# Optimization experiments

Hardware: AMD Instinct MI355X
Metric: run time of the kernel (lower is better)

The kernel has to match this reference:

```python
import jax, jax.numpy as jnp
import numpy as np

DIM = 512
HEADS = 8
DIM_HEAD = 64  # default dim_head used for scale, matches DIM//HEADS here
SCALE = DIM_HEAD ** -0.5
B, X, Y = 8, 32, 32


def setup_inputs() -> dict:
    key = jax.random.key(0)
    k0, k1, k2, k3 = jax.random.split(key, 4)
    fmap = jax.random.normal(k0, (B, DIM, X, Y), dtype=jnp.float32)
    # 1x1 convs as matrices: weight [out, in]
    Wqkvl = jax.random.normal(k1, (4 * DIM, DIM), dtype=jnp.float32) * (DIM ** -0.5)
    Wout = jax.random.normal(k2, (DIM, DIM), dtype=jnp.float32) * (DIM ** -0.5)
    bout = jax.random.normal(k3, (DIM,), dtype=jnp.float32) * 0.01
    return {"fmap": fmap, "Wqkvl": Wqkvl, "Wout": Wout, "bout": bout}


def reference(fmap, Wqkvl, Wout, bout):
    b, c, x, y = fmap.shape
    h, d = HEADS, c // HEADS
    n = x * y
    # 1x1 conv projection to q,k,v,L
    qkvL = jnp.einsum('oc,bcxy->boxy', Wqkvl, fmap)  # [b, 4c, x, y]
    q, k, v, L = jnp.split(qkvL, 4, axis=1)
    # 'b (h d) x y -> b h (x y) d'
    def to_tokens(t):
        return t.reshape(b, h, d, n).transpose(0, 1, 3, 2)
    q, k, v, L = map(to_tokens, (q, k, v, L))
    dots = jnp.einsum('bhid,bhjd->bhij', q, k) * SCALE  # [b,h,n,n]
    attn = jax.nn.softmax(dots, axis=-1)
    out = jnp.einsum('bhij,bhjd->bhid', attn, v) + L  # [b,h,n,d]
    # 'b h (x y) d -> b (h d) x y'
    out = out.transpose(0, 1, 3, 2).reshape(b, c, x, y)
    # output 1x1 conv with bias (dropout=0 -> identity)
    out = jnp.einsum('oc,bcxy->boxy', Wout, out) + bout[None, :, None, None]
    return out
```

## Files before the change

kernel.cpp:

```cpp
#include <hip/hip_runtime.h>

#define Bn 8
#define Cn 512
#define Hn 8
#define Dn 64
#define Nn 1024
#define SCALEQ 0.125f

typedef unsigned short u16;
typedef unsigned short u16x8 __attribute__((ext_vector_type(8)));
typedef unsigned short u16x4 __attribute__((ext_vector_type(4)));
typedef short s16x4 __attribute__((ext_vector_type(4)));
typedef float f32x4 __attribute__((ext_vector_type(4)));
typedef __bf16 bf16x8 __attribute__((ext_vector_type(8)));

__device__ __forceinline__ u16 f2bf(float f){
  unsigned u = __float_as_uint(f);
  u += 0x7fffu + ((u >> 16) & 1u);
  return (u16)(u >> 16);
}
__device__ __forceinline__ float bf2f(u16 h){
  return __uint_as_float(((unsigned)h) << 16);
}
__device__ __forceinline__ f32x4 mfma16(u16x8 a, u16x8 b, f32x4 c){
  return __builtin_amdgcn_mfma_f32_16x16x32_bf16(
      __builtin_bit_cast(bf16x8, a), __builtin_bit_cast(bf16x8, b), c, 0, 0, 0);
}
__device__ __forceinline__ f32x4 mfma16k16(u16x4 a, u16x4 b, f32x4 c){
  return __builtin_amdgcn_mfma_f32_16x16x16bf16_1k(
      __builtin_bit_cast(s16x4, a), __builtin_bit_cast(s16x4, b), c, 0, 0, 0);
}

__device__ __forceinline__ void gload16(const u16* src, u16* dst){
  __builtin_amdgcn_global_load_lds(
      (const __attribute__((address_space(1))) unsigned int*)src,
      (__attribute__((address_space(3))) unsigned int*)dst, 16, 0, 0);
}

__global__ __launch_bounds__(256) void k_convert(const float* __restrict__ src,
                                                 u16* __restrict__ dst, int n4){
  int i = blockIdx.x * 256 + threadIdx.x;
  if (i >= n4) return;
  float4 f = reinterpret_cast<const float4*>(src)[i];
  u16x4 o;
  o[0] = f2bf(f.x); o[1] = f2bf(f.y); o[2] = f2bf(f.z); o[3] = f2bf(f.w);
  reinterpret_cast<u16x4*>(dst)[i] = o;
}

__global__ __launch_bounds__(256) void k_transpose(const float* __restrict__ fmap,
                                                   u16* __restrict__ fmapT){
  __shared__ float tile[32][33];
  const int n0 = blockIdx.x * 32, c0 = blockIdx.y * 32, b = blockIdx.z;
  const int tx = threadIdx.x & 31, ty = threadIdx.x >> 5;
  const float* src = fmap + ((size_t)b * Cn + c0) * Nn + n0;
#pragma unroll
  for (int i = 0; i < 4; i++) tile[ty + 8*i][tx] = src[(size_t)(ty + 8*i) * Nn + tx];
  __syncthreads();
  u16* dst = fmapT + ((size_t)b * Nn + n0) * Cn + c0;
#pragma unroll
  for (int i = 0; i < 4; i++) dst[(size_t)(ty + 8*i) * Cn + tx] = f2bf(tile[tx][ty + 8*i]);
}

__device__ __forceinline__ void stage64(const u16* g, size_t ldg, u16* lbase, int w, int lane){
#pragma unroll
  for (int s = 0; s < 2; s++){
    int row = s*32 + w*8 + (lane>>3);
    const u16* src = g + (size_t)row*ldg + (((lane&7) ^ (row&7)) * 8);
    u16* dst = lbase + (s*32 + w*8)*64;
    gload16(src, dst);
  }
}
__device__ __forceinline__ void stage128x32(const u16* g, size_t ldg, u16* lbase, int w, int lane){
#pragma unroll
  for (int s = 0; s < 2; s++){
    int row = s*64 + w*16 + (lane>>2);
    const u16* src = g + (size_t)row*ldg + (((lane&3) ^ (row&3)) * 8);
    u16* dst = lbase + (s*64 + w*16)*32;
    gload16(src, dst);
  }
}

__device__ __forceinline__ void gemm_fma(const u16x8 (&af)[4], const u16x8 (&bf)[4],
                                         f32x4 (&acc)[4][4]){
#pragma unroll
  for (int i = 0; i < 4; i++)
#pragma unroll
    for (int j = 0; j < 4; j++)
      acc[i][j] = mfma16(af[i], bf[j], acc[i][j]);
}

__device__ __forceinline__ void gemm_nt_128(const u16* __restrict__ Ap, int lda,
                                            const u16* __restrict__ Bp, int ldb,
                                            u16* sA, u16* sB,
                                            f32x4 (&acc)[4][4]){
  const int tid = threadIdx.x;
  const int w = tid >> 6, lane = tid & 63, r = lane & 15, g = lane >> 4;
  const int wi = w >> 1, wj = w & 1;
  stage128x32(Ap, lda, sA, w, lane);
  stage128x32(Bp, ldb, sB, w, lane);
  for (int ks = 0; ks < Cn/32; ks++){
    __syncthreads();
    const int cur = ks & 1;
    if (ks + 1 < Cn/32){
      stage128x32(Ap + (ks+1)*32, lda, sA + (cur^1)*128*32, w, lane);
      stage128x32(Bp + (ks+1)*32, ldb, sB + (cur^1)*128*32, w, lane);
    }
    const u16* Al = sA + cur*128*32;
    const u16* Bl = sB + cur*128*32;
    u16x8 af[4], bf[4];
#pragma unroll
    for (int t = 0; t < 4; t++){
      int ar = wi*64 + t*16 + r;
      af[t] = *reinterpret_cast<const u16x8*>(&Al[ar*32 + ((g ^ (ar&3)) * 8)]);
      int br = wj*64 + t*16 + r;
      bf[t] = *reinterpret_cast<const u16x8*>(&Bl[br*32 + ((g ^ (br&3)) * 8)]);
    }
    gemm_fma(af, bf, acc);
  }
}

__global__ __launch_bounds__(256) void k_gemm1(const u16* __restrict__ fmapT,
                                               const u16* __restrict__ W1,
                                               u16* __restrict__ Qb, u16* __restrict__ Kb,
                                               u16* __restrict__ Vt, u16* __restrict__ Lb){
  __shared__ u16 sA[2*128*32], sB[2*128*32];
  const int ob = blockIdx.x;
  const int nb = blockIdx.y;
  const int b  = blockIdx.z;
  const int w = threadIdx.x >> 6, wi = w >> 1, wj = w & 1;
  const int lane = threadIdx.x & 63, r = lane & 15, g = lane >> 4;
  const int seg = ob >> 2;

  f32x4 acc[4][4];
  const f32x4 z = {0.f, 0.f, 0.f, 0.f};
#pragma unroll
  for (int i = 0; i < 4; i++)
#pragma unroll
    for (int j = 0; j < 4; j++) acc[i][j] = z;

  const u16* fbase = fmapT + (size_t)b * Nn * Cn;

  if (seg != 2){
    gemm_nt_128(fbase + (size_t)(nb*128) * Cn, Cn, W1 + (size_t)(ob*128) * Cn, Cn, sA, sB, acc);
    u16* dst = (seg == 0) ? Qb : (seg == 1 ? Kb : Lb);
    const float sc = (seg == 0) ? SCALEQ : 1.0f;
#pragma unroll
    for (int it = 0; it < 4; it++)
#pragma unroll
      for (int jt = 0; jt < 4; jt++)
#pragma unroll
        for (int rr = 0; rr < 4; rr++){
          int n = nb*128 + wi*64 + it*16 + 4*g + rr;
          int o = ob*128 + wj*64 + jt*16 + r;
          dst[((size_t)b * Nn + n) * Cn + (o & 511)] = f2bf(acc[it][jt][rr] * sc);
        }
  } else {
    gemm_nt_128(W1 + (size_t)(ob*128) * Cn, Cn, fbase + (size_t)(nb*128) * Cn, Cn, sA, sB, acc);
#pragma unroll
    for (int it = 0; it < 4; it++)
#pragma unroll
      for (int jt = 0; jt < 4; jt++)
#pragma unroll
        for (int rr = 0; rr < 4; rr++){
          int o = ob*128 + wi*64 + it*16 + 4*g + rr;
          int oo = o - 1024;
          int h = oo >> 6, d = oo & 63;
          int n = nb*128 + wj*64 + jt*16 + r;
          Vt[(((size_t)b * Hn + h) * Dn + d) * Nn + n] = f2bf(acc[it][jt][rr]);
        }
  }
}

__global__ __launch_bounds__(256) void k_attn(const u16* __restrict__ Qb,
                                              const u16* __restrict__ Kb,
                                              const u16* __restrict__ Vt,
                                              const u16* __restrict__ Lb,
                                              u16* __restrict__ tok){
  __shared__ u16 Kl[2*64*64], Vl[2*64*64];
  const int bid = blockIdx.x;
  const int w0 = (bid & 7) * 128 + (bid >> 3);
  const int qblk = w0 & 15, h = (w0 >> 4) & 7, b = w0 >> 7;
  const int w = threadIdx.x >> 6, lane = threadIdx.x & 63;
  const int r = lane & 15, g = lane >> 4;
  const int q0 = qblk * 64 + w * 16;

  const u16* qrow = Qb + ((size_t)b * Nn + q0 + r) * Cn + h * Dn + 8 * g;
  u16x8 qf0 = *reinterpret_cast<const u16x8*>(qrow);
  u16x8 qf1 = *reinterpret_cast<const u16x8*>(qrow + 32);

  const u16* kbase = Kb + (size_t)b * Nn * Cn + h * Dn;
  const u16* vbase = Vt + ((size_t)b * Hn + h) * Dn * Nn;

  f32x4 accO[4];
  const f32x4 z = {0.f, 0.f, 0.f, 0.f};
#pragma unroll
  for (int dt = 0; dt < 4; dt++) accO[dt] = z;
  float m = -1e30f, lsum = 0.f;

  stage64(kbase, Cn, Kl, w, lane);
  stage64(vbase, Nn, Vl, w, lane);

  for (int tile = 0; tile < 16; tile++){
    __syncthreads();
    const int cur = tile & 1;
    if (tile + 1 < 16){
      stage64(kbase + (size_t)(tile+1)*64*Cn, Cn, Kl + (cur^1)*64*64, w, lane);
      stage64(vbase + (tile+1)*64,            Nn, Vl + (cur^1)*64*64, w, lane);
    }
    const u16* Kc = Kl + cur*64*64;
    const u16* Vc = Vl + cur*64*64;

    f32x4 st[4];
#pragma unroll
    for (int t = 0; t < 4; t++){
      int row = 16*t + r;
      u16x8 k0 = *reinterpret_cast<const u16x8*>(&Kc[row*64 + ((g       ^ (r&7)) * 8)]);
      u16x8 k1 = *reinterpret_cast<const u16x8*>(&Kc[row*64 + (((4+g)   ^ (r&7)) * 8)]);
      st[t] = mfma16(k0, qf0, z);
      st[t] = mfma16(k1, qf1, st[t]);
    }
    float tm = -1e30f;
#pragma unroll
    for (int t = 0; t < 4; t++)
      tm = fmaxf(tm, fmaxf(fmaxf(st[t][0], st[t][1]), fmaxf(st[t][2], st[t][3])));
    tm = fmaxf(tm, __shfl_xor(tm, 16));
    tm = fmaxf(tm, __shfl_xor(tm, 32));
    if (__any(tm - m > 8.f)){
      float mn = fmaxf(m, tm);
      float al = __expf(m - mn);
      m = mn;
      lsum *= al;
#pragma unroll
      for (int dt = 0; dt < 4; dt++) accO[dt] *= al;
    }
    u16x4 p[4];
    float ls = 0.f;
#pragma unroll
    for (int t = 0; t < 4; t++){
#pragma unroll
      for (int j = 0; j < 4; j++){
        float e = __expf(st[t][j] - m);
        ls += e;
        p[t][j] = f2bf(e);
      }
    }
    lsum += ls;
#pragma unroll
    for (int s = 0; s < 4; s++)
#pragma unroll
      for (int dt = 0; dt < 4; dt++){
        int row = dt*16 + r;
        u16x4 vf = *reinterpret_cast<const u16x4*>(
            &Vc[row*64 + (((2*s + (g>>1)) ^ (r&7)) * 8) + (g&1)*4]);
        accO[dt] = mfma16k16(vf, p[s], accO[dt]);
      }
  }

  lsum += __shfl_xor(lsum, 16);
  lsum += __shfl_xor(lsum, 32);
  float linv = 1.0f / lsum;
  const int n = q0 + r;
  const u16* lrow = Lb + ((size_t)b * Nn + n) * Cn + h * Dn;
  u16* trow = tok + ((size_t)b * Nn + n) * Cn + h * Dn;
#pragma unroll
  for (int dt = 0; dt < 4; dt++){
    u16x4 lv = *reinterpret_cast<const u16x4*>(lrow + dt*16 + 4*g);
    u16x4 ov;
#pragma unroll
    for (int rr = 0; rr < 4; rr++)
      ov[rr] = f2bf(accO[dt][rr] * linv + bf2f(lv[rr]));
    *reinterpret_cast<u16x4*>(trow + dt*16 + 4*g) = ov;
  }
}

__global__ __launch_bounds__(256) void k_gemm2(const u16* __restrict__ tok,
                                               const u16* __restrict__ Wo,
                                               const float* __restrict__ bout,
                                               float* __restrict__ out){
  __shared__ u16 sA[2*128*32], sB[2*128*32];
  const int ob = blockIdx.x;
  const int nb = blockIdx.y;
  const int b  = blockIdx.z;
  const int w = threadIdx.x >> 6, wi = w >> 1, wj = w & 1;
  const int lane = threadIdx.x & 63, r = lane & 15, g = lane >> 4;

  f32x4 acc[4][4];
  const f32x4 z = {0.f, 0.f, 0.f, 0.f};
#pragma unroll
  for (int i = 0; i < 4; i++)
#pragma unroll
    for (int j = 0; j < 4; j++) acc[i][j] = z;

  gemm_nt_128(Wo + (size_t)(ob*128) * Cn, Cn,
              tok + (size_t)b * Nn * Cn + (size_t)(nb*128) * Cn, Cn, sA, sB, acc);

#pragma unroll
  for (int it = 0; it < 4; it++)
#pragma unroll
    for (int jt = 0; jt < 4; jt++)
#pragma unroll
      for (int rr = 0; rr < 4; rr++){
        int o = ob*128 + wi*64 + it*16 + 4*g + rr;
        int n = nb*128 + wj*64 + jt*16 + r;
        out[((size_t)b * Cn + o) * Nn + n] = acc[it][jt][rr] + bout[o];
      }
}

extern "C" void kernel_launch(void* const* d_in, const int* in_sizes, int n_in,
                              void* d_out, int out_size, void* d_ws, size_t ws_size,
                              hipStream_t stream){
  const float* fmap  = (const float*)d_in[0];
  const float* Wqkvl = (const float*)d_in[1];
  const float* Wout  = (const float*)d_in[2];
  const float* bout  = (const float*)d_in[3];
  float* out = (float*)d_out;

  char* ws = (char*)d_ws;
  size_t off = 0;
  auto alloc = [&](size_t bytes) -> void* {
    void* p = ws + off;
    off += (bytes + 255) & ~(size_t)255;
    return p;
  };
  u16* W1bf  = (u16*)alloc((size_t)4*Cn*Cn*2);
  u16* Wobf  = (u16*)alloc((size_t)Cn*Cn*2);
  u16* fmapT = (u16*)alloc((size_t)Bn*Nn*Cn*2);
  u16* Qb    = (u16*)alloc((size_t)Bn*Nn*Cn*2);
  u16* Kb    = (u16*)alloc((size_t)Bn*Nn*Cn*2);
  u16* Lb    = (u16*)alloc((size_t)Bn*Nn*Cn*2);
  u16* Vt    = (u16*)alloc((size_t)Bn*Hn*Dn*Nn*2);
  u16* tok   = fmapT;

  hipLaunchKernelGGL(k_convert, dim3((4*Cn*Cn/4 + 255)/256), dim3(256), 0, stream,
                     Wqkvl, W1bf, 4*Cn*Cn/4);
  hipLaunchKernelGGL(k_convert, dim3((Cn*Cn/4 + 255)/256), dim3(256), 0, stream,
                     Wout, Wobf, Cn*Cn/4);
  hipLaunchKernelGGL(k_transpose, dim3(Nn/32, Cn/32, Bn), dim3(256), 0, stream, fmap, fmapT);
  hipLaunchKernelGGL(k_gemm1, dim3(16, 8, Bn), dim3(256), 0, stream, fmapT, W1bf, Qb, Kb, Vt, Lb);
  hipLaunchKernelGGL(k_attn, dim3(1024), dim3(256), 0, stream, Qb, Kb, Vt, Lb, tok);
  hipLaunchKernelGGL(k_gemm2, dim3(4, 8, Bn), dim3(256), 0, stream, tok, Wobf, bout, out);
}
```

Measured before the change: 96.43 us.

## Process two query tiles per attention block and compute row sums via MFMA

Each attention workgroup now handles 128 queries instead of 64: every wave owns two 16-row query groups that share each staged K/V tile, halving the K/V loads from global memory and LDS per query. The softmax row sum moves from scalar adds plus shuffles onto MFMA using a ones vector, and the probabilities are converted with a native bf16 cast. The grid shrinks to 512 blocks with launch bounds of 2, and the two weight-conversion launches are merged into one kernel. In exchange, register pressure rises and there are fewer blocks to spread across the CUs.

```diff
diff --git a/kernel.cpp b/kernel.cpp
--- a/kernel.cpp
+++ b/kernel.cpp
@@ -37,14 +37,18 @@
       (__attribute__((address_space(3))) unsigned int*)dst, 16, 0, 0);
 }
 
-__global__ __launch_bounds__(256) void k_convert(const float* __restrict__ src,
-                                                 u16* __restrict__ dst, int n4){
+__global__ __launch_bounds__(256) void k_convert2(const float* __restrict__ s1,
+                                                  const float* __restrict__ s2,
+                                                  u16* __restrict__ d1, u16* __restrict__ d2,
+                                                  int n1, int n2){
   int i = blockIdx.x * 256 + threadIdx.x;
-  if (i >= n4) return;
-  float4 f = reinterpret_cast<const float4*>(src)[i];
+  const float* s; u16* d; int j;
+  if (i < n1){ s = s1; d = d1; j = i; }
+  else { if (i >= n1 + n2) return; s = s2; d = d2; j = i - n1; }
+  float4 f = reinterpret_cast<const float4*>(s)[j];
   u16x4 o;
   o[0] = f2bf(f.x); o[1] = f2bf(f.y); o[2] = f2bf(f.z); o[3] = f2bf(f.w);
-  reinterpret_cast<u16x4*>(dst)[i] = o;
+  reinterpret_cast<u16x4*>(d)[j] = o;
 }
 
 __global__ __launch_bounds__(256) void k_transpose(const float* __restrict__ fmap,
@@ -171,105 +175,137 @@
   }
 }
 
-__global__ __launch_bounds__(256) void k_attn(const u16* __restrict__ Qb,
-                                              const u16* __restrict__ Kb,
-                                              const u16* __restrict__ Vt,
-                                              const u16* __restrict__ Lb,
-                                              u16* __restrict__ tok){
+__device__ __forceinline__ void attn_tile(const u16* Kc, const u16* Vc,
+                                          const u16* kbase, const u16* vbase, int next,
+                                          u16* Kn, u16* Vn,
+                                          int w, int lane, int r, int g,
+                                          u16x8 qA0, u16x8 qA1, u16x8 qB0, u16x8 qB1,
+                                          float& mA, float& mB,
+                                          f32x4 (&accA)[4], f32x4 (&accB)[4],
+                                          f32x4& accSA, f32x4& accSB){
+  const f32x4 z = {0.f, 0.f, 0.f, 0.f};
+  __syncthreads();
+  if (next < 16){
+    stage64(kbase + (size_t)next*64*Cn, Cn, Kn, w, lane);
+    stage64(vbase + next*64,            Nn, Vn, w, lane);
+  }
+  f32x4 sA[4], sB[4];
+#pragma unroll
+  for (int t = 0; t < 4; t++){
+    int row = 16*t + r;
+    u16x8 k0 = *reinterpret_cast<const u16x8*>(&Kc[row*64 + ((g       ^ (r&7)) * 8)]);
+    u16x8 k1 = *reinterpret_cast<const u16x8*>(&Kc[row*64 + (((4+g)   ^ (r&7)) * 8)]);
+    sA[t] = mfma16(k0, qA0, z); sA[t] = mfma16(k1, qA1, sA[t]);
+    sB[t] = mfma16(k0, qB0, z); sB[t] = mfma16(k1, qB1, sB[t]);
+  }
+  float tmA = -1e30f, tmB = -1e30f;
+#pragma unroll
+  for (int t = 0; t < 4; t++){
+    tmA = fmaxf(tmA, fmaxf(fmaxf(sA[t][0], sA[t][1]), fmaxf(sA[t][2], sA[t][3])));
+    tmB = fmaxf(tmB, fmaxf(fmaxf(sB[t][0], sB[t][1]), fmaxf(sB[t][2], sB[t][3])));
+  }
+  tmA = fmaxf(tmA, __shfl_xor(tmA, 16)); tmA = fmaxf(tmA, __shfl_xor(tmA, 32));
+  tmB = fmaxf(tmB, __shfl_xor(tmB, 16)); tmB = fmaxf(tmB, __shfl_xor(tmB, 32));
+  if (__any(tmA - mA > 8.f)){
+    float mn = fmaxf(mA, tmA), al = __expf(mA - mn);
+    mA = mn; accSA *= al;
+#pragma unroll
+    for (int dt = 0; dt < 4; dt++) accA[dt] *= al;
+  }
+  if (__any(tmB - mB > 8.f)){
+    float mn = fmaxf(mB, tmB), al = __expf(mB - mn);
+    mB = mn; accSB *= al;
+#pragma unroll
+    for (int dt = 0; dt < 4; dt++) accB[dt] *= al;
+  }
+  u16x4 pA[4], pB[4];
+#pragma unroll
+  for (int t = 0; t < 4; t++){
+#pragma unroll
+    for (int j = 0; j < 4; j++){
+      pA[t][j] = __builtin_bit_cast(u16, (__bf16)__expf(sA[t][j] - mA));
+      pB[t][j] = __builtin_bit_cast(u16, (__bf16)__expf(sB[t][j] - mB));
+    }
+  }
+  const u16x4 ones = {0x3F80u, 0x3F80u, 0x3F80u, 0x3F80u};
+#pragma unroll
+  for (int t = 0; t < 4; t++){
+    accSA = mfma16k16(ones, pA[t], accSA);
+    accSB = mfma16k16(ones, pB[t], accSB);
+  }
+#pragma unroll
+  for (int s = 0; s < 4; s++)
+#pragma unroll
+    for (int dt = 0; dt < 4; dt++){
+      int row = dt*16 + r;
+      u16x4 vf = *reinterpret_cast<const u16x4*>(
+          &Vc[row*64 + (((2*s + (g>>1)) ^ (r&7)) * 8) + (g&1)*4]);
+      accA[dt] = mfma16k16(vf, pA[s], accA[dt]);
+      accB[dt] = mfma16k16(vf, pB[s], accB[dt]);
+    }
+}
+
+__global__ __launch_bounds__(256, 2) void k_attn(const u16* __restrict__ Qb,
+                                                 const u16* __restrict__ Kb,
+                                                 const u16* __restrict__ Vt,
+                                                 const u16* __restrict__ Lb,
+                                                 u16* __restrict__ tok){
   __shared__ u16 Kl[2*64*64], Vl[2*64*64];
   const int bid = blockIdx.x;
-  const int w0 = (bid & 7) * 128 + (bid >> 3);
-  const int qblk = w0 & 15, h = (w0 >> 4) & 7, b = w0 >> 7;
+  const int w0 = (bid & 7) * 64 + (bid >> 3);
+  const int qblk = w0 & 7, h = (w0 >> 3) & 7, b = w0 >> 6;
   const int w = threadIdx.x >> 6, lane = threadIdx.x & 63;
   const int r = lane & 15, g = lane >> 4;
-  const int q0 = qblk * 64 + w * 16;
-
-  const u16* qrow = Qb + ((size_t)b * Nn + q0 + r) * Cn + h * Dn + 8 * g;
-  u16x8 qf0 = *reinterpret_cast<const u16x8*>(qrow);
-  u16x8 qf1 = *reinterpret_cast<const u16x8*>(qrow + 32);
+  const int qA = qblk * 128 + w * 16;
+  const int qB = qA + 64;
+
+  const u16* qrowA = Qb + ((size_t)b * Nn + qA + r) * Cn + h * Dn + 8 * g;
+  const u16* qrowB = Qb + ((size_t)b * Nn + qB + r) * Cn + h * Dn + 8 * g;
+  u16x8 qA0 = *reinterpret_cast<const u16x8*>(qrowA);
+  u16x8 qA1 = *reinterpret_cast<const u16x8*>(qrowA + 32);
+  u16x8 qB0 = *reinterpret_cast<const u16x8*>(qrowB);
+  u16x8 qB1 = *reinterpret_cast<const u16x8*>(qrowB + 32);
 
   const u16* kbase = Kb + (size_t)b * Nn * Cn + h * Dn;
   const u16* vbase = Vt + ((size_t)b * Hn + h) * Dn * Nn;
 
-  f32x4 accO[4];
+  f32x4 accA[4], accB[4];
   const f32x4 z = {0.f, 0.f, 0.f, 0.f};
 #pragma unroll
-  for (int dt = 0; dt < 4; dt++) accO[dt] = z;
-  float m = -1e30f, lsum = 0.f;
-
-  stage64(kbase, Cn, Kl, w, lane);
-  stage64(vbase, Nn, Vl, w, lane);
-
-  for (int tile = 0; tile < 16; tile++){
-    __syncthreads();
-    const int cur = tile & 1;
-    if (tile + 1 < 16){
-      stage64(kbase + (size_t)(tile+1)*64*Cn, Cn, Kl + (cur^1)*64*64, w, lane);
-      stage64(vbase + (tile+1)*64,            Nn, Vl + (cur^1)*64*64, w, lane);
-    }
-    const u16* Kc = Kl + cur*64*64;
-    const u16* Vc = Vl + cur*64*64;
-
-    f32x4 st[4];
-#pragma unroll
-    for (int t = 0; t < 4; t++){
-      int row = 16*t + r;
-      u16x8 k0 = *reinterpret_cast<const u16x8*>(&Kc[row*64 + ((g       ^ (r&7)) * 8)]);
-      u16x8 k1 = *reinterpret_cast<const u16x8*>(&Kc[row*64 + (((4+g)   ^ (r&7)) * 8)]);
-      st[t] = mfma16(k0, qf0, z);
-      st[t] = mfma16(k1, qf1, st[t]);
-    }
-    float tm = -1e30f;
-#pragma unroll
-    for (int t = 0; t < 4; t++)
-      tm = fmaxf(tm, fmaxf(fmaxf(st[t][0], st[t][1]), fmaxf(st[t][2], st[t][3])));
-    tm = fmaxf(tm, __shfl_xor(tm, 16));
-    tm = fmaxf(tm, __shfl_xor(tm, 32));
-    if (__any(tm - m > 8.f)){
-      float mn = fmaxf(m, tm);
-      float al = __expf(m - mn);
-      m = mn;
-      lsum *= al;
-#pragma unroll
-      for (int dt = 0; dt < 4; dt++) accO[dt] *= al;
-    }
-    u16x4 p[4];
-    float ls = 0.f;
-#pragma unroll
-    for (int t = 0; t < 4; t++){
-#pragma unroll
-      for (int j = 0; j < 4; j++){
-        float e = __expf(st[t][j] - m);
-        ls += e;
-        p[t][j] = f2bf(e);
-      }
-    }
-    lsum += ls;
-#pragma unroll
-    for (int s = 0; s < 4; s++)
-#pragma unroll
-      for (int dt = 0; dt < 4; dt++){
-        int row = dt*16 + r;
-        u16x4 vf = *reinterpret_cast<const u16x4*>(
-            &Vc[row*64 + (((2*s + (g>>1)) ^ (r&7)) * 8) + (g&1)*4]);
-        accO[dt] = mfma16k16(vf, p[s], accO[dt]);
-      }
-  }
-
-  lsum += __shfl_xor(lsum, 16);
-  lsum += __shfl_xor(lsum, 32);
-  float linv = 1.0f / lsum;
-  const int n = q0 + r;
-  const u16* lrow = Lb + ((size_t)b * Nn + n) * Cn + h * Dn;
-  u16* trow = tok + ((size_t)b * Nn + n) * Cn + h * Dn;
-#pragma unroll
-  for (int dt = 0; dt < 4; dt++){
-    u16x4 lv = *reinterpret_cast<const u16x4*>(lrow + dt*16 + 4*g);
-    u16x4 ov;
-#pragma unroll
-    for (int rr = 0; rr < 4; rr++)
-      ov[rr] = f2bf(accO[dt][rr] * linv + bf2f(lv[rr]));
-    *reinterpret_cast<u16x4*>(trow + dt*16 + 4*g) = ov;
+  for (int dt = 0; dt < 4; dt++){ accA[dt] = z; accB[dt] = z; }
+  f32x4 accSA = z, accSB = z;
+  float mA = -1e30f, mB = -1e30f;
+
+  u16* Kl0 = Kl, *Kl1 = Kl + 64*64;
+  u16* Vl0 = Vl, *Vl1 = Vl + 64*64;
+  stage64(kbase, Cn, Kl0, w, lane);
+  stage64(vbase, Nn, Vl0, w, lane);
+
+  for (int tile = 0; tile < 16; tile += 2){
+    attn_tile(Kl0, Vl0, kbase, vbase, tile + 1, Kl1, Vl1, w, lane, r, g,
+              qA0, qA1, qB0, qB1, mA, mB, accA, accB, accSA, accSB);
+    attn_tile(Kl1, Vl1, kbase, vbase, tile + 2, Kl0, Vl0, w, lane, r, g,
+              qA0, qA1, qB0, qB1, mA, mB, accA, accB, accSA, accSB);
+  }
+
+  float linvA = 1.0f / accSA[0];
+  float linvB = 1.0f / accSB[0];
+#pragma unroll
+  for (int half = 0; half < 2; half++){
+    const int n = (half ? qB : qA) + r;
+    const float linv = half ? linvB : linvA;
+    const f32x4* acc = half ? accB : accA;
+    const u16* lrow = Lb + ((size_t)b * Nn + n) * Cn + h * Dn;
+    u16* trow = tok + ((size_t)b * Nn + n) * Cn + h * Dn;
+#pragma unroll
+    for (int dt = 0; dt < 4; dt++){
+      u16x4 lv = *reinterpret_cast<const u16x4*>(lrow + dt*16 + 4*g);
+      u16x4 ov;
+#pragma unroll
+      for (int rr = 0; rr < 4; rr++)
+        ov[rr] = f2bf(acc[dt][rr] * linv + bf2f(lv[rr]));
+      *reinterpret_cast<u16x4*>(trow + dt*16 + 4*g) = ov;
+    }
   }
 }
 
@@ -331,12 +367,11 @@
   u16* Vt    = (u16*)alloc((size_t)Bn*Hn*Dn*Nn*2);
   u16* tok   = fmapT;
 
-  hipLaunchKernelGGL(k_convert, dim3((4*Cn*Cn/4 + 255)/256), dim3(256), 0, stream,
-                     Wqkvl, W1bf, 4*Cn*Cn/4);
-  hipLaunchKernelGGL(k_convert, dim3((Cn*Cn/4 + 255)/256), dim3(256), 0, stream,
-                     Wout, Wobf, Cn*Cn/4);
+  const int n1 = 4*Cn*Cn/4, n2 = Cn*Cn/4;
+  hipLaunchKernelGGL(k_convert2, dim3((n1 + n2 + 255)/256), dim3(256), 0, stream,
+                     Wqkvl, Wout, W1bf, Wobf, n1, n2);
   hipLaunchKernelGGL(k_transpose, dim3(Nn/32, Cn/32, Bn), dim3(256), 0, stream, fmap, fmapT);
   hipLaunchKernelGGL(k_gemm1, dim3(16, 8, Bn), dim3(256), 0, stream, fmapT, W1bf, Qb, Kb, Vt, Lb);
-  hipLaunchKernelGGL(k_attn, dim3(1024), dim3(256), 0, stream, Qb, Kb, Vt, Lb, tok);
+  hipLaunchKernelGGL(k_attn, dim3(512), dim3(256), 0, stream, Qb, Kb, Vt, Lb, tok);
   hipLaunchKernelGGL(k_gemm2, dim3(4, 8, Bn), dim3(256), 0, stream, tok, Wobf, bout, out);
 }
```

New measurement: 90.29 us. 6.4% less time.
